# Performance work log

Measured on AMD Instinct MI355X. Metric: run time of the kernel, lower is better.

Reference implementation:

```python
import jax, jax.numpy as jnp
import numpy as np
from jax import lax

VOCAB, NUM_CLASSES = 21128, 53
EMB, FILT, K = 128, 128, 3
B, L = 512, 512


def setup_inputs() -> dict:
    key = jax.random.key(0)
    ks = jax.random.split(key, 8)
    char_ids = jax.random.randint(ks[0], (B, L), 0, VOCAB, dtype=jnp.int64 if jax.config.jax_enable_x64 else jnp.int32)
    pos_e1 = jax.random.randint(ks[1], (B,), 0, L - 1, dtype=jnp.int32)
    pos_e2 = jax.random.randint(ks[2], (B,), 0, L - 1, dtype=jnp.int32)
    emb_table = jax.random.normal(ks[3], (VOCAB, EMB), dtype=jnp.float32) * 0.02
    emb_table = emb_table.at[0].set(0.0)  # padding_idx=0
    conv_w = jax.random.normal(ks[4], (FILT, EMB, K), dtype=jnp.float32) * (1.0 / np.sqrt(EMB * K))
    conv_b = jax.random.normal(ks[5], (FILT,), dtype=jnp.float32) * 0.01
    fc_w = jax.random.normal(ks[6], (NUM_CLASSES, FILT * 3), dtype=jnp.float32) * (1.0 / np.sqrt(FILT * 3))
    fc_b = jax.random.normal(ks[7], (NUM_CLASSES,), dtype=jnp.float32) * 0.01
    return {"char_ids": char_ids, "pos_e1": pos_e1, "pos_e2": pos_e2,
            "emb_table": emb_table, "conv_w": conv_w, "conv_b": conv_b,
            "fc_w": fc_w, "fc_b": fc_b}


def reference(char_ids, pos_e1, pos_e2, emb_table, conv_w, conv_b, fc_w, fc_b):
    b, seq = char_ids.shape
    x = emb_table[char_ids]                      # (b, L, E)
    x = jnp.transpose(x, (0, 2, 1))              # (b, E, L)
    conv_out = lax.conv_general_dilated(
        x, conv_w, window_strides=(1,), padding=[(K // 2, K // 2)],
        dimension_numbers=("NCH", "OIH", "NCH"))
    conv_out = jax.nn.relu(conv_out + conv_b[None, :, None])  # (b, F, L)

    # sort + clip entity boundaries, replicate e1==e2 -> e2=e1+1 adjustment
    e1 = jnp.clip(jnp.minimum(pos_e1, pos_e2), 0, seq)
    e2 = jnp.clip(jnp.maximum(pos_e1, pos_e2), 0, seq)
    e2 = jnp.where(e1 == e2, jnp.minimum(e1 + 1, seq), e2)

    idx = jnp.arange(seq)[None, :]               # (1, L)
    m1 = idx < jnp.maximum(e1, 1)[:, None]       # [:e1] or [:1] if e1==0
    m2 = (idx >= e1[:, None]) & (idx < e2[:, None])
    m3 = idx >= jnp.minimum(e2, seq - 1)[:, None]  # [e2:] or last col if e2==L

    neg = jnp.float32(-jnp.inf)
    def seg_max(mask):
        return jnp.max(jnp.where(mask[:, None, :], conv_out, neg), axis=-1)  # (b, F)

    pooled = jnp.concatenate([seg_max(m1), seg_max(m2), seg_max(m3)], axis=-1)  # (b, 3F)
    return pooled @ fc_w.T + fc_b
```

## Files before the change

kernel.cpp:

```cpp
#include <hip/hip_runtime.h>
#include <stdint.h>

#define VOCAB 21128
#define NUMC  53
#define EMB   128
#define SEQ   512
#define BATCH 512

typedef __bf16 bf16x8 __attribute__((ext_vector_type(8)));
typedef float f32x4 __attribute__((ext_vector_type(4)));

__device__ __forceinline__ unsigned int f2bf1(float f) {
    union { float f; unsigned int u; } v; v.f = f;
    return (v.u + 0x7FFFu + ((v.u >> 16) & 1u)) >> 16;
}
__device__ __forceinline__ unsigned int pack2(float a, float b) {
    return f2bf1(a) | (f2bf1(b) << 16);
}
__device__ __forceinline__ float b2f(unsigned short u) {
    union { float f; unsigned int i; } v; v.i = ((unsigned int)u) << 16; return v.f;
}

__global__ void prep_kernel(const float* __restrict__ emb, const float* __restrict__ cw,
                            unsigned short* __restrict__ Tb, unsigned short* __restrict__ Wp) {
    int idx = blockIdx.x * blockDim.x + threadIdx.x;
    const int n8 = VOCAB * EMB / 8;
    if (idx < n8) {
        const float4* src = (const float4*)emb + (size_t)idx * 2;
        float4 a = src[0], b = src[1];
        uint4 o;
        o.x = pack2(a.x, a.y);
        o.y = pack2(a.z, a.w);
        o.z = pack2(b.x, b.y);
        o.w = pack2(b.z, b.w);
        *(uint4*)(Tb + (size_t)idx * 8) = o;
    }
    if (idx < 12 * 8 * 64 * 8) {
        int j = idx & 7, l = (idx >> 3) & 63, g = (idx >> 9) & 7, s = idx >> 12;
        int kk = s * 32 + (l >> 4) * 8 + j;
        int f = g * 16 + (l & 15);
        int tap = kk >> 7, e = kk & 127;
        Wp[idx] = (unsigned short)f2bf1(cw[(f * EMB + e) * 3 + tap]);
    }
}

__launch_bounds__(256)
__global__ void pcnn_vgemm(const unsigned short* __restrict__ Tb,
                           const unsigned short* __restrict__ Wp,
                           unsigned short* __restrict__ P) {
    const int tid  = threadIdx.x;
    const int lane = tid & 63;
    const int wn   = tid >> 6;
    const int quad = lane >> 4;
    const int lc   = lane & 15;
    const int row0 = blockIdx.x * 64;

    f32x4 acc[3][4][2];
#pragma unroll
    for (int t = 0; t < 3; ++t)
#pragma unroll
        for (int mt = 0; mt < 4; ++mt)
#pragma unroll
            for (int nt = 0; nt < 2; ++nt)
                acc[t][mt][nt] = (f32x4){0.f, 0.f, 0.f, 0.f};

#pragma unroll
    for (int s = 0; s < 12; ++s) {
        const int tap = s >> 2;
        const int q   = (s & 3) * 4 + quad;
        bf16x8 b0 = *(const bf16x8*)(Wp + (size_t)((s * 8 + wn * 2) * 64 + lane) * 8);
        bf16x8 b1 = *(const bf16x8*)(Wp + (size_t)((s * 8 + wn * 2 + 1) * 64 + lane) * 8);
#pragma unroll
        for (int mt = 0; mt < 4; ++mt) {
            bf16x8 a = *(const bf16x8*)(Tb + (size_t)(row0 + mt * 16 + lc) * 128 + q * 8);
            acc[tap][mt][0] = __builtin_amdgcn_mfma_f32_16x16x32_bf16(a, b0, acc[tap][mt][0], 0, 0, 0);
            acc[tap][mt][1] = __builtin_amdgcn_mfma_f32_16x16x32_bf16(a, b1, acc[tap][mt][1], 0, 0, 0);
        }
    }

#pragma unroll
    for (int tap = 0; tap < 3; ++tap)
#pragma unroll
        for (int mt = 0; mt < 4; ++mt) {
            int grb = row0 + mt * 16 + quad * 4;
#pragma unroll
            for (int nt = 0; nt < 2; ++nt) {
                int col = tap * 128 + (wn * 2 + nt) * 16 + lc;
#pragma unroll
                for (int reg = 0; reg < 4; ++reg) {
                    int gr = grb + reg;
                    if (gr < VOCAB)
                        P[(size_t)gr * 384 + col] = (unsigned short)f2bf1(acc[tap][mt][nt][reg]);
                }
            }
        }
}

__launch_bounds__(256)
__global__ void pcnn_gather(const int* __restrict__ cid, const int* __restrict__ p1,
                            const int* __restrict__ p2,
                            const unsigned short* __restrict__ P,
                            float* __restrict__ Pd) {
    __shared__ int idsB[130];
    __shared__ float pstage[2][3][128];

    const int bx  = blockIdx.x;
    const int b   = bx >> 2;
    const int tq  = bx & 3;
    const int tid = threadIdx.x;

    const int* crow = cid + (size_t)b * SEQ;
    if (tid < 130) {
        int p = tq * 128 + tid - 1;
        unsigned int id = (p >= 0 && p < SEQ) ? (unsigned int)crow[p] : 0u;
        idsB[tid] = (int)(id * 768u);
    }

    int e1 = min(p1[b], p2[b]);
    int e2 = max(p1[b], p2[b]);
    if (e1 == e2) e2 = min(e1 + 1, SEQ);
    const int e1m = max(e1, 1);

    __syncthreads();

    const int f    = tid & 127;
    const int half = tid >> 7;
    const char* Pb = (const char*)P;
    const int o0 = f * 2;
    const int o1 = 256 + f * 2;
    const int o2 = 512 + f * 2;

    float smax0 = -1e30f, smax1 = -1e30f, smax2 = -1e30f;

#pragma unroll 4
    for (int pass = 0; pass < 64; ++pass) {
        int ll = pass * 2 + half;
        int p  = tq * 128 + ll;
        float v = b2f(*(const unsigned short*)(Pb + idsB[ll]     + o0))
                + b2f(*(const unsigned short*)(Pb + idsB[ll + 1] + o1))
                + b2f(*(const unsigned short*)(Pb + idsB[ll + 2] + o2));
        smax0 = fmaxf(smax0, v + ((p < e1m)           ? 0.f : -2e30f));
        smax1 = fmaxf(smax1, v + ((p >= e1 && p < e2) ? 0.f : -2e30f));
        smax2 = fmaxf(smax2, v + ((p >= e2)           ? 0.f : -2e30f));
    }

    pstage[half][0][f] = smax0;
    pstage[half][1][f] = smax1;
    pstage[half][2][f] = smax2;
    __syncthreads();

    for (int j = tid; j < 384; j += 256) {
        int s3 = j >> 7, ff = j & 127;
        Pd[((size_t)b * 4 + tq) * 384 + j] = fmaxf(pstage[0][s3][ff], pstage[1][s3][ff]);
    }
}

__launch_bounds__(256)
__global__ void pcnn_combine(const float* __restrict__ Pd, const float* __restrict__ cb,
                             const float* __restrict__ fcw, const float* __restrict__ fcb,
                             float* __restrict__ out) {
    __shared__ float pooled[384];
    __shared__ float fcred[NUMC][4];
    const int b = blockIdx.x;
    const int tid = threadIdx.x;

    for (int j = tid; j < 384; j += 256) {
        const float* pp = Pd + (size_t)b * 4 * 384 + j;
        float m = fmaxf(fmaxf(pp[0], pp[384]), fmaxf(pp[768], pp[1152]));
        pooled[j] = fmaxf(m + cb[j & 127], 0.f);
    }
    __syncthreads();

    if (tid < 212) {
        int c = tid >> 2, q = tid & 3;
        const float* wrow = fcw + (size_t)c * 384 + q * 96;
        const float* pp   = pooled + q * 96;
        float sum = 0.f;
#pragma unroll 8
        for (int i = 0; i < 96; ++i) sum += wrow[i] * pp[i];
        fcred[c][q] = sum;
    }
    __syncthreads();
    if (tid < NUMC)
        out[(size_t)b * NUMC + tid] =
            fcred[tid][0] + fcred[tid][1] + fcred[tid][2] + fcred[tid][3] + fcb[tid];
}

extern "C" void kernel_launch(void* const* d_in, const int* in_sizes, int n_in,
                              void* d_out, int out_size, void* d_ws, size_t ws_size,
                              hipStream_t stream) {
    const int*   cid = (const int*)d_in[0];
    const int*   p1  = (const int*)d_in[1];
    const int*   p2  = (const int*)d_in[2];
    const float* emb = (const float*)d_in[3];
    const float* cw  = (const float*)d_in[4];
    const float* cb  = (const float*)d_in[5];
    const float* fcw = (const float*)d_in[6];
    const float* fcb = (const float*)d_in[7];
    float* out = (float*)d_out;

    unsigned short* Tb = (unsigned short*)d_ws;
    unsigned short* Wp = (unsigned short*)((char*)d_ws + (size_t)VOCAB * EMB * 2);
    unsigned short* P  = (unsigned short*)((char*)d_ws + (size_t)VOCAB * EMB * 2 + 98304);
    float*          Pd = (float*)((char*)d_ws + (size_t)VOCAB * EMB * 2 + 98304
                                  + (size_t)VOCAB * 384 * 2);

    const int n8 = VOCAB * EMB / 8;
    const int prep_threads = 256;
    const int prep_blocks  = (n8 + prep_threads - 1) / prep_threads;
    const int gemm_blocks  = (VOCAB + 63) / 64;
    prep_kernel<<<prep_blocks, prep_threads, 0, stream>>>(emb, cw, Tb, Wp);
    pcnn_vgemm<<<gemm_blocks, 256, 0, stream>>>(Tb, Wp, P);
    pcnn_gather<<<BATCH * 4, 256, 0, stream>>>(cid, p1, p2, P, Pd);
    pcnn_combine<<<BATCH, 256, 0, stream>>>(Pd, cb, fcw, fcb, out);
}
```

Measured before the change: 122.9 us.

## Fuse embedding bf16 conversion into GEMM and gather with combine

The vocabulary GEMM now converts fp32 embedding rows to bf16 itself and stages them in swizzled shared memory, so the separate full-table conversion pass and its workspace round trip are gone. The gather and FC combine kernels are merged into one 1024-thread block per batch row that reduces eight partial maxima in shared memory, removing the Pd intermediate and a launch. The cost is fewer, larger gather blocks (512 instead of 2048), which lowers parallelism and makes occupancy depend on the 1024-thread block size.

```diff
diff --git a/kernel.cpp b/kernel.cpp
--- a/kernel.cpp
+++ b/kernel.cpp
@@ -21,20 +21,8 @@
     union { float f; unsigned int i; } v; v.i = ((unsigned int)u) << 16; return v.f;
 }
 
-__global__ void prep_kernel(const float* __restrict__ emb, const float* __restrict__ cw,
-                            unsigned short* __restrict__ Tb, unsigned short* __restrict__ Wp) {
+__global__ void prep_w(const float* __restrict__ cw, unsigned short* __restrict__ Wp) {
     int idx = blockIdx.x * blockDim.x + threadIdx.x;
-    const int n8 = VOCAB * EMB / 8;
-    if (idx < n8) {
-        const float4* src = (const float4*)emb + (size_t)idx * 2;
-        float4 a = src[0], b = src[1];
-        uint4 o;
-        o.x = pack2(a.x, a.y);
-        o.y = pack2(a.z, a.w);
-        o.z = pack2(b.x, b.y);
-        o.w = pack2(b.z, b.w);
-        *(uint4*)(Tb + (size_t)idx * 8) = o;
-    }
     if (idx < 12 * 8 * 64 * 8) {
         int j = idx & 7, l = (idx >> 3) & 63, g = (idx >> 9) & 7, s = idx >> 12;
         int kk = s * 32 + (l >> 4) * 8 + j;
@@ -45,9 +33,11 @@
 }
 
 __launch_bounds__(256)
-__global__ void pcnn_vgemm(const unsigned short* __restrict__ Tb,
+__global__ void pcnn_vgemm(const float* __restrict__ emb,
                            const unsigned short* __restrict__ Wp,
                            unsigned short* __restrict__ P) {
+    __shared__ __align__(16) unsigned short As[64 * 128];
+
     const int tid  = threadIdx.x;
     const int lane = tid & 63;
     const int wn   = tid >> 6;
@@ -55,6 +45,22 @@
     const int lc   = lane & 15;
     const int row0 = blockIdx.x * 64;
 
+#pragma unroll
+    for (int i = 0; i < 4; ++i) {
+        int task = tid + 256 * i;
+        int r = task >> 4, c = task & 15;
+        int gr = row0 + r;
+        uint4 o = {0u, 0u, 0u, 0u};
+        if (gr < VOCAB) {
+            const float4* src = (const float4*)(emb + (size_t)gr * EMB + c * 8);
+            float4 a = src[0], b = src[1];
+            o.x = pack2(a.x, a.y); o.y = pack2(a.z, a.w);
+            o.z = pack2(b.x, b.y); o.w = pack2(b.z, b.w);
+        }
+        *(uint4*)((char*)As + (r * 16 + (c ^ (r & 15))) * 16) = o;
+    }
+    __syncthreads();
+
     f32x4 acc[3][4][2];
 #pragma unroll
     for (int t = 0; t < 3; ++t)
@@ -72,7 +78,8 @@
         bf16x8 b1 = *(const bf16x8*)(Wp + (size_t)((s * 8 + wn * 2 + 1) * 64 + lane) * 8);
 #pragma unroll
         for (int mt = 0; mt < 4; ++mt) {
-            bf16x8 a = *(const bf16x8*)(Tb + (size_t)(row0 + mt * 16 + lc) * 128 + q * 8);
+            int r = mt * 16 + lc;
+            bf16x8 a = *(const bf16x8*)(As + r * 128 + (q ^ (r & 15)) * 8);
             acc[tap][mt][0] = __builtin_amdgcn_mfma_f32_16x16x32_bf16(a, b0, acc[tap][mt][0], 0, 0, 0);
             acc[tap][mt][1] = __builtin_amdgcn_mfma_f32_16x16x32_bf16(a, b1, acc[tap][mt][1], 0, 0, 0);
         }
@@ -96,24 +103,27 @@
         }
 }
 
-__launch_bounds__(256)
-__global__ void pcnn_gather(const int* __restrict__ cid, const int* __restrict__ p1,
-                            const int* __restrict__ p2,
-                            const unsigned short* __restrict__ P,
-                            float* __restrict__ Pd) {
-    __shared__ int idsB[130];
-    __shared__ float pstage[2][3][128];
-
-    const int bx  = blockIdx.x;
-    const int b   = bx >> 2;
-    const int tq  = bx & 3;
+__launch_bounds__(1024)
+__global__ void pcnn_gather_fc(const int* __restrict__ cid, const int* __restrict__ p1,
+                               const int* __restrict__ p2,
+                               const unsigned short* __restrict__ P,
+                               const float* __restrict__ cb,
+                               const float* __restrict__ fcw,
+                               const float* __restrict__ fcb,
+                               float* __restrict__ out) {
+    __shared__ int idsB[514];
+    __shared__ float pstage[8][3][128];
+    __shared__ float pooled[384];
+    __shared__ float fcred[NUMC][4];
+
+    const int b   = blockIdx.x;
     const int tid = threadIdx.x;
 
     const int* crow = cid + (size_t)b * SEQ;
-    if (tid < 130) {
-        int p = tq * 128 + tid - 1;
+    for (int i = tid; i < 514; i += 1024) {
+        int p = i - 1;
         unsigned int id = (p >= 0 && p < SEQ) ? (unsigned int)crow[p] : 0u;
-        idsB[tid] = (int)(id * 768u);
+        idsB[i] = (int)(id * 768u);
     }
 
     int e1 = min(p1[b], p2[b]);
@@ -134,11 +144,10 @@
 
 #pragma unroll 4
     for (int pass = 0; pass < 64; ++pass) {
-        int ll = pass * 2 + half;
-        int p  = tq * 128 + ll;
-        float v = b2f(*(const unsigned short*)(Pb + idsB[ll]     + o0))
-                + b2f(*(const unsigned short*)(Pb + idsB[ll + 1] + o1))
-                + b2f(*(const unsigned short*)(Pb + idsB[ll + 2] + o2));
+        int p = pass * 8 + half;
+        float v = b2f(*(const unsigned short*)(Pb + idsB[p]     + o0))
+                + b2f(*(const unsigned short*)(Pb + idsB[p + 1] + o1))
+                + b2f(*(const unsigned short*)(Pb + idsB[p + 2] + o2));
         smax0 = fmaxf(smax0, v + ((p < e1m)           ? 0.f : -2e30f));
         smax1 = fmaxf(smax1, v + ((p >= e1 && p < e2) ? 0.f : -2e30f));
         smax2 = fmaxf(smax2, v + ((p >= e2)           ? 0.f : -2e30f));
@@ -149,25 +158,12 @@
     pstage[half][2][f] = smax2;
     __syncthreads();
 
-    for (int j = tid; j < 384; j += 256) {
-        int s3 = j >> 7, ff = j & 127;
-        Pd[((size_t)b * 4 + tq) * 384 + j] = fmaxf(pstage[0][s3][ff], pstage[1][s3][ff]);
-    }
-}
-
-__launch_bounds__(256)
-__global__ void pcnn_combine(const float* __restrict__ Pd, const float* __restrict__ cb,
-                             const float* __restrict__ fcw, const float* __restrict__ fcb,
-                             float* __restrict__ out) {
-    __shared__ float pooled[384];
-    __shared__ float fcred[NUMC][4];
-    const int b = blockIdx.x;
-    const int tid = threadIdx.x;
-
-    for (int j = tid; j < 384; j += 256) {
-        const float* pp = Pd + (size_t)b * 4 * 384 + j;
-        float m = fmaxf(fmaxf(pp[0], pp[384]), fmaxf(pp[768], pp[1152]));
-        pooled[j] = fmaxf(m + cb[j & 127], 0.f);
+    if (tid < 384) {
+        int s3 = tid >> 7, ff = tid & 127;
+        float m = pstage[0][s3][ff];
+#pragma unroll
+        for (int h = 1; h < 8; ++h) m = fmaxf(m, pstage[h][s3][ff]);
+        pooled[tid] = fmaxf(m + cb[ff], 0.f);
     }
     __syncthreads();
 
@@ -199,18 +195,11 @@
     const float* fcb = (const float*)d_in[7];
     float* out = (float*)d_out;
 
-    unsigned short* Tb = (unsigned short*)d_ws;
-    unsigned short* Wp = (unsigned short*)((char*)d_ws + (size_t)VOCAB * EMB * 2);
-    unsigned short* P  = (unsigned short*)((char*)d_ws + (size_t)VOCAB * EMB * 2 + 98304);
-    float*          Pd = (float*)((char*)d_ws + (size_t)VOCAB * EMB * 2 + 98304
-                                  + (size_t)VOCAB * 384 * 2);
-
-    const int n8 = VOCAB * EMB / 8;
-    const int prep_threads = 256;
-    const int prep_blocks  = (n8 + prep_threads - 1) / prep_threads;
-    const int gemm_blocks  = (VOCAB + 63) / 64;
-    prep_kernel<<<prep_blocks, prep_threads, 0, stream>>>(emb, cw, Tb, Wp);
-    pcnn_vgemm<<<gemm_blocks, 256, 0, stream>>>(Tb, Wp, P);
-    pcnn_gather<<<BATCH * 4, 256, 0, stream>>>(cid, p1, p2, P, Pd);
-    pcnn_combine<<<BATCH, 256, 0, stream>>>(Pd, cb, fcw, fcb, out);
-}
+    unsigned short* Wp = (unsigned short*)d_ws;
+    unsigned short* P  = (unsigned short*)((char*)d_ws + 98304);
+
+    const int gemm_blocks = (VOCAB + 63) / 64;
+    prep_w<<<192, 256, 0, stream>>>(cw, Wp);
+    pcnn_vgemm<<<gemm_blocks, 256, 0, stream>>>(emb, Wp, P);
+    pcnn_gather_fc<<<BATCH, 1024, 0, stream>>>(cid, p1, p2, P, cb, fcw, fcb, out);
+}
```

After: 115.8 us. 5.8% less time.
